# Performance work log

Hardware: AMD Instinct MI355X
Metric: run time of the kernel (lower is better)

Reference implementation:

```python
import jax, jax.numpy as jnp
import numpy as np


def setup_inputs() -> dict:
    key = jax.random.key(0)
    k1, k2, k3 = jax.random.split(key, 3)
    B, H, S, D = 2, 16, 2048, 64
    q = jax.random.normal(k1, (B, H, S, D), dtype=jnp.float32)
    k = jax.random.normal(k2, (B, H, S, D), dtype=jnp.float32)
    v = jax.random.normal(k3, (B, H, S, D), dtype=jnp.float32)
    return {"q": q, "k": k, "v": v}


def reference(q, k, v):
    # q,k,v: [B,H,S,D]; causal attention with 1/sqrt(D) scaling, fp32 softmax.
    scale = 1.0 / (q.shape[-1] ** 0.5)
    scores = jnp.einsum('bhqd,bhkd->bhqk', q * scale, k)  # [B,H,S,S]
    S = scores.shape[-1]
    causal_mask = jnp.triu(jnp.ones((S, S), dtype=bool), k=1)
    scores = jnp.where(causal_mask, -jnp.inf, scores)
    attn = jax.nn.softmax(scores.astype(jnp.float32), axis=-1).astype(q.dtype)
    output = jnp.einsum('bhqk,bhkd->bhqd', attn, v)
    # Module also returns an all-zeros attn_weights placeholder of shape [B,H,S,S]
    attn_weights = jnp.zeros(scores.shape, dtype=q.dtype)
    return (output, attn_weights)
```

## Files before the change

kernel.cpp:

```cpp
#include <hip/hip_runtime.h>


typedef __bf16 bf16x8 __attribute__((ext_vector_type(8)));
typedef float f32x4 __attribute__((ext_vector_type(4)));

#define LOG2E 1.44269504088896340736f

__device__ __forceinline__ unsigned short f2bf(float f) {
  unsigned int u = __float_as_uint(f);
  u += 0x7fffu + ((u >> 16) & 1u);
  return (unsigned short)(u >> 16);
}

__device__ __forceinline__ void block_sync_lds() {
  asm volatile("s_waitcnt lgkmcnt(0)" ::: "memory");
  __builtin_amdgcn_s_barrier();
}

constexpr int Sdim = 2048, Ddim = 64, BHn = 32;
constexpr int STiles = 16;
constexpr int LDK = 72;
constexpr int OUT0 = BHn * Sdim * Ddim;
constexpr size_t FILL_PER_BH = 1048576;

__device__ __forceinline__ int vswz_m(int d) { return ((d >> 2) ^ (d >> 5)) & 7; }

__global__ __launch_bounds__(256, 2)
void flash_causal_kernel(const float* __restrict__ Q, const float* __restrict__ K,
                         const float* __restrict__ V, float* __restrict__ out) {
  __shared__ unsigned short Klds[2][64 * LDK];
  __shared__ unsigned short Vlds[2][64 * LDK];
  __shared__ unsigned short Plds[4][2][16 * LDK];

  const int tid  = threadIdx.x;
  const int wave = tid >> 6;
  const int lane = tid & 63;
  const int quad = lane >> 4;
  const int l15  = lane & 15;

  const int bh = blockIdx.x & (BHn - 1);
  const int g  = (int)(blockIdx.x >> 5);
  const int s  = (g & 1) ? (STiles - 1) - (g >> 1) : (g >> 1);
  const int jmax = 2 * s + 1;

  const int base  = bh * Sdim * Ddim;
  const int qbase = s * 128;

  bf16x8 aq[2][2];
  #pragma unroll
  for (int f = 0; f < 2; ++f) {
    const float* qp = Q + base + (qbase + 64 * f + wave * 16 + l15) * Ddim + quad * 8;
    #pragma unroll
    for (int s2 = 0; s2 < 2; ++s2) {
      float4 a = *(const float4*)(qp + 32 * s2);
      float4 b = *(const float4*)(qp + 32 * s2 + 4);
      union { unsigned short u[8]; bf16x8 v; } u;
      u.u[0] = f2bf(a.x * 0.125f); u.u[1] = f2bf(a.y * 0.125f);
      u.u[2] = f2bf(a.z * 0.125f); u.u[3] = f2bf(a.w * 0.125f);
      u.u[4] = f2bf(b.x * 0.125f); u.u[5] = f2bf(b.y * 0.125f);
      u.u[6] = f2bf(b.z * 0.125f); u.u[7] = f2bf(b.w * 0.125f);
      aq[f][s2] = u.v;
    }
  }

  f32x4 ot[2][4];
  #pragma unroll
  for (int f = 0; f < 2; ++f)
    #pragma unroll
    for (int t = 0; t < 4; ++t) ot[f][t] = (f32x4){0.f, 0.f, 0.f, 0.f};
  float mrun[2] = {-__builtin_inff(), -__builtin_inff()};
  float lrun[2] = {0.f, 0.f};

  const float4* kg4 = (const float4*)(K + base);
  const float4* vg4 = (const float4*)(V + base);
  float4 kf[4], vf[4];

  auto ldtile = [&](int j) {
    const float4* kp = kg4 + j * 1024;
    const float4* vp = vg4 + j * 1024;
    #pragma unroll
    for (int i = 0; i < 4; ++i) { kf[i] = kp[i * 256 + tid]; vf[i] = vp[i * 256 + tid]; }
  };
  auto stage = [&](int buf) {
    #pragma unroll
    for (int i = 0; i < 4; ++i) {
      int lin = i * 256 + tid;
      int row = lin >> 4;
      int c4  = (lin & 15) << 2;
      uint2 t2;
      t2.x = (unsigned int)f2bf(kf[i].x) | ((unsigned int)f2bf(kf[i].y) << 16);
      t2.y = (unsigned int)f2bf(kf[i].z) | ((unsigned int)f2bf(kf[i].w) << 16);
      *(uint2*)&Klds[buf][row * LDK + c4] = t2;
      const int sw = vswz_m(c4) << 3;
      Vlds[buf][(c4 + 0) * LDK + (row ^ sw)] = f2bf(vf[i].x);
      Vlds[buf][(c4 + 1) * LDK + (row ^ sw)] = f2bf(vf[i].y);
      Vlds[buf][(c4 + 2) * LDK + (row ^ sw)] = f2bf(vf[i].z);
      Vlds[buf][(c4 + 3) * LDK + (row ^ sw)] = f2bf(vf[i].w);
    }
  };

  ldtile(0); stage(0); ldtile(1);

  for (int j = 0; j <= jmax; ++j) {
    block_sync_lds();
    if (j < jmax) stage((j + 1) & 1);
    if (j + 2 <= jmax) ldtile(j + 2);

    const unsigned short* Kb = Klds[j & 1];
    const unsigned short* Vb = Vlds[j & 1];
    const bool f0act = (j <= 2 * s);

    f32x4 sc[2][4];
    #pragma unroll
    for (int f = 0; f < 2; ++f)
      #pragma unroll
      for (int t = 0; t < 4; ++t) sc[f][t] = (f32x4){0.f, 0.f, 0.f, 0.f};
    __builtin_amdgcn_s_setprio(1);
    #pragma unroll
    for (int s2 = 0; s2 < 2; ++s2) {
      #pragma unroll
      for (int t = 0; t < 4; ++t) {
        bf16x8 ka = *(const bf16x8*)&Kb[(16 * t + l15) * LDK + 32 * s2 + quad * 8];
        sc[0][t] = __builtin_amdgcn_mfma_f32_16x16x32_bf16(ka, aq[0][s2], sc[0][t], 0, 0, 0);
        sc[1][t] = __builtin_amdgcn_mfma_f32_16x16x32_bf16(ka, aq[1][s2], sc[1][t], 0, 0, 0);
      }
    }
    __builtin_amdgcn_s_setprio(0);

    #pragma unroll
    for (int f = 0; f < 2; ++f) {
      if (j == 2 * s + f) {
        const int qml = wave * 16 + l15;
        #pragma unroll
        for (int t = 0; t < 4; ++t)
          #pragma unroll
          for (int r = 0; r < 4; ++r)
            if (16 * t + 4 * quad + r > qml) sc[f][t][r] = -__builtin_inff();
      }
    }

    #pragma unroll
    for (int f = 0; f < 2; ++f) {
      if (f == 0 && !f0act) continue;
      float mx = sc[f][0][0];
      #pragma unroll
      for (int t = 0; t < 4; ++t)
        #pragma unroll
        for (int r = 0; r < 4; ++r) mx = fmaxf(mx, sc[f][t][r]);
      mx = fmaxf(mx, __shfl_xor(mx, 16));
      mx = fmaxf(mx, __shfl_xor(mx, 32));
      float mn    = fmaxf(mrun[f], mx);
      float alpha = __builtin_amdgcn_exp2f((mrun[f] - mn) * LOG2E);
      float msc   = mn * LOG2E;
      mrun[f] = mn;
      float rs = 0.f;
      #pragma unroll
      for (int t = 0; t < 4; ++t)
        #pragma unroll
        for (int r = 0; r < 4; ++r) {
          float p = __builtin_amdgcn_exp2f(fmaf(sc[f][t][r], LOG2E, -msc));
          sc[f][t][r] = p;
          rs += p;
        }
      rs += __shfl_xor(rs, 16);
      rs += __shfl_xor(rs, 32);
      lrun[f] = lrun[f] * alpha + rs;
      #pragma unroll
      for (int t = 0; t < 4; ++t)
        #pragma unroll
        for (int r = 0; r < 4; ++r) ot[f][t][r] *= alpha;
      #pragma unroll
      for (int t = 0; t < 4; ++t) {
        uint2 pw;
        pw.x = (unsigned int)f2bf(sc[f][t][0]) | ((unsigned int)f2bf(sc[f][t][1]) << 16);
        pw.y = (unsigned int)f2bf(sc[f][t][2]) | ((unsigned int)f2bf(sc[f][t][3]) << 16);
        *(uint2*)&Plds[wave][f][l15 * LDK + 16 * t + 4 * quad] = pw;
      }
    }

    __builtin_amdgcn_s_setprio(1);
    #pragma unroll
    for (int s2 = 0; s2 < 2; ++s2) {
      bf16x8 pb0, pb1;
      if (f0act) pb0 = *(const bf16x8*)&Plds[wave][0][l15 * LDK + 32 * s2 + quad * 8];
      pb1 = *(const bf16x8*)&Plds[wave][1][l15 * LDK + 32 * s2 + quad * 8];
      #pragma unroll
      for (int t = 0; t < 4; ++t) {
        const int d = 16 * t + l15;
        bf16x8 va = *(const bf16x8*)&Vb[d * LDK + (((4 * s2 + quad) ^ vswz_m(d)) << 3)];
        if (f0act)
          ot[0][t] = __builtin_amdgcn_mfma_f32_16x16x32_bf16(va, pb0, ot[0][t], 0, 0, 0);
        ot[1][t] = __builtin_amdgcn_mfma_f32_16x16x32_bf16(va, pb1, ot[1][t], 0, 0, 0);
      }
    }
    __builtin_amdgcn_s_setprio(0);
  }

  #pragma unroll
  for (int f = 0; f < 2; ++f) {
    float inv = 1.0f / lrun[f];
    float* orow = out + base + (qbase + 64 * f + wave * 16 + l15) * Ddim + 4 * quad;
    #pragma unroll
    for (int t = 0; t < 4; ++t) {
      f32x4 o4;
      o4.x = ot[f][t][0] * inv; o4.y = ot[f][t][1] * inv;
      o4.z = ot[f][t][2] * inv; o4.w = ot[f][t][3] * inv;
      *(f32x4*)(orow + 16 * t) = o4;
    }
  }

  {
    const int gp = (STiles - 1) - s;
    const int w  = 2 * gp + 1;
    const size_t start_f4 = (size_t)bh * FILL_PER_BH + (size_t)4096 * (gp * gp);
    const size_t count_f4 = (size_t)4096 * w;
    f32x4 z4 = (f32x4){0.f, 0.f, 0.f, 0.f};
    f32x4* zp = (f32x4*)(out + OUT0) + start_f4;
    for (size_t i = tid; i < count_f4; i += 256)
      __builtin_nontemporal_store(z4, zp + i);
  }
}

extern "C" void kernel_launch(void* const* d_in, const int* in_sizes, int n_in,
                              void* d_out, int out_size, void* d_ws, size_t ws_size,
                              hipStream_t stream) {
  const float* q = (const float*)d_in[0];
  const float* k = (const float*)d_in[1];
  const float* v = (const float*)d_in[2];
  float* out = (float*)d_out;
  dim3 grid(BHn * STiles);
  flash_causal_kernel<<<grid, dim3(256), 0, stream>>>(q, k, v, out);
}
```

Before: 586.6 us.

## Split zero-fill into dedicated blocks interleaved with attention blocks

The grid becomes 768 blocks, and every third block only writes its contiguous share of the all-zero attention-weights output. The other two in each group run the attention tiles, so attention blocks no longer carry a trailing zero-fill tail of uneven size. Launch bounds rise to three blocks per CU, and the P scratch buffer uses a tighter stride to cut LDS use. The aim is to overlap the write-bandwidth-bound fill with compute-bound attention across CUs. The cost is possible register pressure or spills under the tighter occupancy bound.

```diff
diff --git a/kernel.cpp b/kernel.cpp
--- a/kernel.cpp
+++ b/kernel.cpp
@@ -20,26 +20,42 @@
 constexpr int Sdim = 2048, Ddim = 64, BHn = 32;
 constexpr int STiles = 16;
 constexpr int LDK = 72;
+constexpr int LDP = 68;
 constexpr int OUT0 = BHn * Sdim * Ddim;
-constexpr size_t FILL_PER_BH = 1048576;
+constexpr size_t FILL_F4_PER_BLK = 131072;
 
 __device__ __forceinline__ int vswz_m(int d) { return ((d >> 2) ^ (d >> 5)) & 7; }
 
-__global__ __launch_bounds__(256, 2)
+__global__ __launch_bounds__(256, 3)
 void flash_causal_kernel(const float* __restrict__ Q, const float* __restrict__ K,
                          const float* __restrict__ V, float* __restrict__ out) {
   __shared__ unsigned short Klds[2][64 * LDK];
   __shared__ unsigned short Vlds[2][64 * LDK];
-  __shared__ unsigned short Plds[4][2][16 * LDK];
-
-  const int tid  = threadIdx.x;
+  __shared__ unsigned short Plds[4][2][16 * LDP];
+
+  const int tid = threadIdx.x;
+  const int b   = (int)blockIdx.x;
+  const int bmod = b - (b / 3) * 3;
+
+  if (bmod == 2) {
+    const int fidx = b / 3;
+    f32x4* zp = (f32x4*)(out + OUT0) + (size_t)fidx * FILL_F4_PER_BLK;
+    const f32x4 z4 = (f32x4){0.f, 0.f, 0.f, 0.f};
+    #pragma unroll 4
+    for (size_t i = tid; i < FILL_F4_PER_BLK; i += 256)
+      __builtin_nontemporal_store(z4, zp + i);
+    return;
+  }
+
+  const int c = (b / 3) * 2 + bmod;
+
   const int wave = tid >> 6;
   const int lane = tid & 63;
   const int quad = lane >> 4;
   const int l15  = lane & 15;
 
-  const int bh = blockIdx.x & (BHn - 1);
-  const int g  = (int)(blockIdx.x >> 5);
+  const int bh = c & (BHn - 1);
+  const int g  = c >> 5;
   const int s  = (g & 1) ? (STiles - 1) - (g >> 1) : (g >> 1);
   const int jmax = 2 * s + 1;
 
@@ -53,12 +69,12 @@
     #pragma unroll
     for (int s2 = 0; s2 < 2; ++s2) {
       float4 a = *(const float4*)(qp + 32 * s2);
-      float4 b = *(const float4*)(qp + 32 * s2 + 4);
+      float4 bq = *(const float4*)(qp + 32 * s2 + 4);
       union { unsigned short u[8]; bf16x8 v; } u;
-      u.u[0] = f2bf(a.x * 0.125f); u.u[1] = f2bf(a.y * 0.125f);
-      u.u[2] = f2bf(a.z * 0.125f); u.u[3] = f2bf(a.w * 0.125f);
-      u.u[4] = f2bf(b.x * 0.125f); u.u[5] = f2bf(b.y * 0.125f);
-      u.u[6] = f2bf(b.z * 0.125f); u.u[7] = f2bf(b.w * 0.125f);
+      u.u[0] = f2bf(a.x * 0.125f);  u.u[1] = f2bf(a.y * 0.125f);
+      u.u[2] = f2bf(a.z * 0.125f);  u.u[3] = f2bf(a.w * 0.125f);
+      u.u[4] = f2bf(bq.x * 0.125f); u.u[5] = f2bf(bq.y * 0.125f);
+      u.u[6] = f2bf(bq.z * 0.125f); u.u[7] = f2bf(bq.w * 0.125f);
       aq[f][s2] = u.v;
     }
   }
@@ -174,7 +190,7 @@
         uint2 pw;
         pw.x = (unsigned int)f2bf(sc[f][t][0]) | ((unsigned int)f2bf(sc[f][t][1]) << 16);
         pw.y = (unsigned int)f2bf(sc[f][t][2]) | ((unsigned int)f2bf(sc[f][t][3]) << 16);
-        *(uint2*)&Plds[wave][f][l15 * LDK + 16 * t + 4 * quad] = pw;
+        *(uint2*)&Plds[wave][f][l15 * LDP + 16 * t + 4 * quad] = pw;
       }
     }
 
@@ -182,8 +198,8 @@
     #pragma unroll
     for (int s2 = 0; s2 < 2; ++s2) {
       bf16x8 pb0, pb1;
-      if (f0act) pb0 = *(const bf16x8*)&Plds[wave][0][l15 * LDK + 32 * s2 + quad * 8];
-      pb1 = *(const bf16x8*)&Plds[wave][1][l15 * LDK + 32 * s2 + quad * 8];
+      if (f0act) pb0 = *(const bf16x8*)&Plds[wave][0][l15 * LDP + 32 * s2 + quad * 8];
+      pb1 = *(const bf16x8*)&Plds[wave][1][l15 * LDP + 32 * s2 + quad * 8];
       #pragma unroll
       for (int t = 0; t < 4; ++t) {
         const int d = 16 * t + l15;
@@ -207,17 +223,6 @@
       o4.z = ot[f][t][2] * inv; o4.w = ot[f][t][3] * inv;
       *(f32x4*)(orow + 16 * t) = o4;
     }
-  }
-
-  {
-    const int gp = (STiles - 1) - s;
-    const int w  = 2 * gp + 1;
-    const size_t start_f4 = (size_t)bh * FILL_PER_BH + (size_t)4096 * (gp * gp);
-    const size_t count_f4 = (size_t)4096 * w;
-    f32x4 z4 = (f32x4){0.f, 0.f, 0.f, 0.f};
-    f32x4* zp = (f32x4*)(out + OUT0) + start_f4;
-    for (size_t i = tid; i < count_f4; i += 256)
-      __builtin_nontemporal_store(z4, zp + i);
   }
 }
 
@@ -228,6 +233,6 @@
   const float* k = (const float*)d_in[1];
   const float* v = (const float*)d_in[2];
   float* out = (float*)d_out;
-  dim3 grid(BHn * STiles);
+  dim3 grid(768);
   flash_causal_kernel<<<grid, dim3(256), 0, stream>>>(q, k, v, out);
 }
```

After: 654.5 us. +11.6%, slower.

## Enlarge tiles to 256-query blocks with 512 threads and 128-key tiles

Applied to the files above, without the earlier changes.

Each block now handles 256 query rows with 8 waves of 512 threads and consumes 128-key K/V tiles, so the grid shrinks to 256 blocks. The larger tiles give more reuse of each staged K/V tile and fewer barriers per key. The cost is more registers per thread (the score tile doubles) and more masked work on the diagonal. The grid now has exactly one block per CU with coarse, uneven causal work, because the interleaved load-balancing order of query tiles was dropped. This risks tail imbalance and lower occupancy.

```diff
diff --git a/kernel.cpp b/kernel.cpp
--- a/kernel.cpp
+++ b/kernel.cpp
@@ -18,19 +18,22 @@
 }
 
 constexpr int Sdim = 2048, Ddim = 64, BHn = 32;
-constexpr int STiles = 16;
+constexpr int QTiles = 8;
 constexpr int LDK = 72;
+constexpr int LDV = 136;
+constexpr int LDP = 136;
 constexpr int OUT0 = BHn * Sdim * Ddim;
 constexpr size_t FILL_PER_BH = 1048576;
+constexpr int FILL_UNIT_F4 = 16384;
 
 __device__ __forceinline__ int vswz_m(int d) { return ((d >> 2) ^ (d >> 5)) & 7; }
 
-__global__ __launch_bounds__(256, 2)
+__global__ __launch_bounds__(512, 2)
 void flash_causal_kernel(const float* __restrict__ Q, const float* __restrict__ K,
                          const float* __restrict__ V, float* __restrict__ out) {
-  __shared__ unsigned short Klds[2][64 * LDK];
-  __shared__ unsigned short Vlds[2][64 * LDK];
-  __shared__ unsigned short Plds[4][2][16 * LDK];
+  __shared__ unsigned short Klds[2][128 * LDK];
+  __shared__ unsigned short Vlds[2][64 * LDV];
+  __shared__ unsigned short Plds[8][2][16 * LDP];
 
   const int tid  = threadIdx.x;
   const int wave = tid >> 6;
@@ -38,27 +41,26 @@
   const int quad = lane >> 4;
   const int l15  = lane & 15;
 
-  const int bh = blockIdx.x & (BHn - 1);
-  const int g  = (int)(blockIdx.x >> 5);
-  const int s  = (g & 1) ? (STiles - 1) - (g >> 1) : (g >> 1);
-  const int jmax = 2 * s + 1;
+  const int bh = (int)blockIdx.x & (BHn - 1);
+  const int t  = (int)blockIdx.x >> 5;
+  const int jmax = 2 * t + 1;
 
   const int base  = bh * Sdim * Ddim;
-  const int qbase = s * 128;
+  const int qbase = t * 256;
 
   bf16x8 aq[2][2];
   #pragma unroll
   for (int f = 0; f < 2; ++f) {
-    const float* qp = Q + base + (qbase + 64 * f + wave * 16 + l15) * Ddim + quad * 8;
+    const float* qp = Q + base + (qbase + 32 * wave + 16 * f + l15) * Ddim + quad * 8;
     #pragma unroll
     for (int s2 = 0; s2 < 2; ++s2) {
       float4 a = *(const float4*)(qp + 32 * s2);
-      float4 b = *(const float4*)(qp + 32 * s2 + 4);
+      float4 bq = *(const float4*)(qp + 32 * s2 + 4);
       union { unsigned short u[8]; bf16x8 v; } u;
-      u.u[0] = f2bf(a.x * 0.125f); u.u[1] = f2bf(a.y * 0.125f);
-      u.u[2] = f2bf(a.z * 0.125f); u.u[3] = f2bf(a.w * 0.125f);
-      u.u[4] = f2bf(b.x * 0.125f); u.u[5] = f2bf(b.y * 0.125f);
-      u.u[6] = f2bf(b.z * 0.125f); u.u[7] = f2bf(b.w * 0.125f);
+      u.u[0] = f2bf(a.x * 0.125f);  u.u[1] = f2bf(a.y * 0.125f);
+      u.u[2] = f2bf(a.z * 0.125f);  u.u[3] = f2bf(a.w * 0.125f);
+      u.u[4] = f2bf(bq.x * 0.125f); u.u[5] = f2bf(bq.y * 0.125f);
+      u.u[6] = f2bf(bq.z * 0.125f); u.u[7] = f2bf(bq.w * 0.125f);
       aq[f][s2] = u.v;
     }
   }
@@ -67,7 +69,7 @@
   #pragma unroll
   for (int f = 0; f < 2; ++f)
     #pragma unroll
-    for (int t = 0; t < 4; ++t) ot[f][t] = (f32x4){0.f, 0.f, 0.f, 0.f};
+    for (int tt = 0; tt < 4; ++tt) ot[f][tt] = (f32x4){0.f, 0.f, 0.f, 0.f};
   float mrun[2] = {-__builtin_inff(), -__builtin_inff()};
   float lrun[2] = {0.f, 0.f};
 
@@ -76,15 +78,15 @@
   float4 kf[4], vf[4];
 
   auto ldtile = [&](int j) {
-    const float4* kp = kg4 + j * 1024;
-    const float4* vp = vg4 + j * 1024;
-    #pragma unroll
-    for (int i = 0; i < 4; ++i) { kf[i] = kp[i * 256 + tid]; vf[i] = vp[i * 256 + tid]; }
+    const float4* kp = kg4 + j * 2048;
+    const float4* vp = vg4 + j * 2048;
+    #pragma unroll
+    for (int i = 0; i < 4; ++i) { kf[i] = kp[i * 512 + tid]; vf[i] = vp[i * 512 + tid]; }
   };
   auto stage = [&](int buf) {
     #pragma unroll
     for (int i = 0; i < 4; ++i) {
-      int lin = i * 256 + tid;
+      int lin = i * 512 + tid;
       int row = lin >> 4;
       int c4  = (lin & 15) << 2;
       uint2 t2;
@@ -92,10 +94,10 @@
       t2.y = (unsigned int)f2bf(kf[i].z) | ((unsigned int)f2bf(kf[i].w) << 16);
       *(uint2*)&Klds[buf][row * LDK + c4] = t2;
       const int sw = vswz_m(c4) << 3;
-      Vlds[buf][(c4 + 0) * LDK + (row ^ sw)] = f2bf(vf[i].x);
-      Vlds[buf][(c4 + 1) * LDK + (row ^ sw)] = f2bf(vf[i].y);
-      Vlds[buf][(c4 + 2) * LDK + (row ^ sw)] = f2bf(vf[i].z);
-      Vlds[buf][(c4 + 3) * LDK + (row ^ sw)] = f2bf(vf[i].w);
+      Vlds[buf][(c4 + 0) * LDV + (row ^ sw)] = f2bf(vf[i].x);
+      Vlds[buf][(c4 + 1) * LDV + (row ^ sw)] = f2bf(vf[i].y);
+      Vlds[buf][(c4 + 2) * LDV + (row ^ sw)] = f2bf(vf[i].z);
+      Vlds[buf][(c4 + 3) * LDV + (row ^ sw)] = f2bf(vf[i].w);
     }
   };
 
@@ -108,45 +110,43 @@
 
     const unsigned short* Kb = Klds[j & 1];
     const unsigned short* Vb = Vlds[j & 1];
-    const bool f0act = (j <= 2 * s);
-
-    f32x4 sc[2][4];
+
+    f32x4 sc[2][8];
     #pragma unroll
     for (int f = 0; f < 2; ++f)
       #pragma unroll
-      for (int t = 0; t < 4; ++t) sc[f][t] = (f32x4){0.f, 0.f, 0.f, 0.f};
+      for (int tt = 0; tt < 8; ++tt) sc[f][tt] = (f32x4){0.f, 0.f, 0.f, 0.f};
     __builtin_amdgcn_s_setprio(1);
     #pragma unroll
     for (int s2 = 0; s2 < 2; ++s2) {
       #pragma unroll
-      for (int t = 0; t < 4; ++t) {
-        bf16x8 ka = *(const bf16x8*)&Kb[(16 * t + l15) * LDK + 32 * s2 + quad * 8];
-        sc[0][t] = __builtin_amdgcn_mfma_f32_16x16x32_bf16(ka, aq[0][s2], sc[0][t], 0, 0, 0);
-        sc[1][t] = __builtin_amdgcn_mfma_f32_16x16x32_bf16(ka, aq[1][s2], sc[1][t], 0, 0, 0);
+      for (int tt = 0; tt < 8; ++tt) {
+        bf16x8 ka = *(const bf16x8*)&Kb[(16 * tt + l15) * LDK + 32 * s2 + quad * 8];
+        sc[0][tt] = __builtin_amdgcn_mfma_f32_16x16x32_bf16(ka, aq[0][s2], sc[0][tt], 0, 0, 0);
+        sc[1][tt] = __builtin_amdgcn_mfma_f32_16x16x32_bf16(ka, aq[1][s2], sc[1][tt], 0, 0, 0);
       }
     }
     __builtin_amdgcn_s_setprio(0);
 
-    #pragma unroll
-    for (int f = 0; f < 2; ++f) {
-      if (j == 2 * s + f) {
-        const int qml = wave * 16 + l15;
-        #pragma unroll
-        for (int t = 0; t < 4; ++t)
+    if (j >= 2 * t) {
+      #pragma unroll
+      for (int f = 0; f < 2; ++f) {
+        const int qml = 32 * wave + 16 * f + l15 - ((j - 2 * t) << 7);
+        #pragma unroll
+        for (int tt = 0; tt < 8; ++tt)
           #pragma unroll
           for (int r = 0; r < 4; ++r)
-            if (16 * t + 4 * quad + r > qml) sc[f][t][r] = -__builtin_inff();
+            if (16 * tt + 4 * quad + r > qml) sc[f][tt][r] = -__builtin_inff();
       }
     }
 
     #pragma unroll
     for (int f = 0; f < 2; ++f) {
-      if (f == 0 && !f0act) continue;
       float mx = sc[f][0][0];
       #pragma unroll
-      for (int t = 0; t < 4; ++t)
-        #pragma unroll
-        for (int r = 0; r < 4; ++r) mx = fmaxf(mx, sc[f][t][r]);
+      for (int tt = 0; tt < 8; ++tt)
+        #pragma unroll
+        for (int r = 0; r < 4; ++r) mx = fmaxf(mx, sc[f][tt][r]);
       mx = fmaxf(mx, __shfl_xor(mx, 16));
       mx = fmaxf(mx, __shfl_xor(mx, 32));
       float mn    = fmaxf(mrun[f], mx);
@@ -155,42 +155,40 @@
       mrun[f] = mn;
       float rs = 0.f;
       #pragma unroll
-      for (int t = 0; t < 4; ++t)
+      for (int tt = 0; tt < 8; ++tt)
         #pragma unroll
         for (int r = 0; r < 4; ++r) {
-          float p = __builtin_amdgcn_exp2f(fmaf(sc[f][t][r], LOG2E, -msc));
-          sc[f][t][r] = p;
+          float p = __builtin_amdgcn_exp2f(fmaf(sc[f][tt][r], LOG2E, -msc));
+          sc[f][tt][r] = p;
           rs += p;
         }
       rs += __shfl_xor(rs, 16);
       rs += __shfl_xor(rs, 32);
       lrun[f] = lrun[f] * alpha + rs;
       #pragma unroll
-      for (int t = 0; t < 4; ++t)
-        #pragma unroll
-        for (int r = 0; r < 4; ++r) ot[f][t][r] *= alpha;
-      #pragma unroll
-      for (int t = 0; t < 4; ++t) {
+      for (int tt = 0; tt < 4; ++tt)
+        #pragma unroll
+        for (int r = 0; r < 4; ++r) ot[f][tt][r] *= alpha;
+      #pragma unroll
+      for (int tt = 0; tt < 8; ++tt) {
         uint2 pw;
-        pw.x = (unsigned int)f2bf(sc[f][t][0]) | ((unsigned int)f2bf(sc[f][t][1]) << 16);
-        pw.y = (unsigned int)f2bf(sc[f][t][2]) | ((unsigned int)f2bf(sc[f][t][3]) << 16);
-        *(uint2*)&Plds[wave][f][l15 * LDK + 16 * t + 4 * quad] = pw;
+        pw.x = (unsigned int)f2bf(sc[f][tt][0]) | ((unsigned int)f2bf(sc[f][tt][1]) << 16);
+        pw.y = (unsigned int)f2bf(sc[f][tt][2]) | ((unsigned int)f2bf(sc[f][tt][3]) << 16);
+        *(uint2*)&Plds[wave][f][l15 * LDP + 16 * tt + 4 * quad] = pw;
       }
     }
 
     __builtin_amdgcn_s_setprio(1);
     #pragma unroll
-    for (int s2 = 0; s2 < 2; ++s2) {
-      bf16x8 pb0, pb1;
-      if (f0act) pb0 = *(const bf16x8*)&Plds[wave][0][l15 * LDK + 32 * s2 + quad * 8];
-      pb1 = *(const bf16x8*)&Plds[wave][1][l15 * LDK + 32 * s2 + quad * 8];
-      #pragma unroll
-      for (int t = 0; t < 4; ++t) {
-        const int d = 16 * t + l15;
-        bf16x8 va = *(const bf16x8*)&Vb[d * LDK + (((4 * s2 + quad) ^ vswz_m(d)) << 3)];
-        if (f0act)
-          ot[0][t] = __builtin_amdgcn_mfma_f32_16x16x32_bf16(va, pb0, ot[0][t], 0, 0, 0);
-        ot[1][t] = __builtin_amdgcn_mfma_f32_16x16x32_bf16(va, pb1, ot[1][t], 0, 0, 0);
+    for (int ks = 0; ks < 4; ++ks) {
+      bf16x8 pb0 = *(const bf16x8*)&Plds[wave][0][l15 * LDP + 32 * ks + quad * 8];
+      bf16x8 pb1 = *(const bf16x8*)&Plds[wave][1][l15 * LDP + 32 * ks + quad * 8];
+      #pragma unroll
+      for (int tt = 0; tt < 4; ++tt) {
+        const int d = 16 * tt + l15;
+        bf16x8 va = *(const bf16x8*)&Vb[d * LDV + (((4 * ks + quad) ^ vswz_m(d)) << 3)];
+        ot[0][tt] = __builtin_amdgcn_mfma_f32_16x16x32_bf16(va, pb0, ot[0][tt], 0, 0, 0);
+        ot[1][tt] = __builtin_amdgcn_mfma_f32_16x16x32_bf16(va, pb1, ot[1][tt], 0, 0, 0);
       }
     }
     __builtin_amdgcn_s_setprio(0);
@@ -199,24 +197,23 @@
   #pragma unroll
   for (int f = 0; f < 2; ++f) {
     float inv = 1.0f / lrun[f];
-    float* orow = out + base + (qbase + 64 * f + wave * 16 + l15) * Ddim + 4 * quad;
-    #pragma unroll
-    for (int t = 0; t < 4; ++t) {
+    float* orow = out + base + (qbase + 32 * wave + 16 * f + l15) * Ddim + 4 * quad;
+    #pragma unroll
+    for (int tt = 0; tt < 4; ++tt) {
       f32x4 o4;
-      o4.x = ot[f][t][0] * inv; o4.y = ot[f][t][1] * inv;
-      o4.z = ot[f][t][2] * inv; o4.w = ot[f][t][3] * inv;
-      *(f32x4*)(orow + 16 * t) = o4;
+      o4.x = ot[f][tt][0] * inv; o4.y = ot[f][tt][1] * inv;
+      o4.z = ot[f][tt][2] * inv; o4.w = ot[f][tt][3] * inv;
+      *(f32x4*)(orow + 16 * tt) = o4;
     }
   }
 
   {
-    const int gp = (STiles - 1) - s;
-    const int w  = 2 * gp + 1;
-    const size_t start_f4 = (size_t)bh * FILL_PER_BH + (size_t)4096 * (gp * gp);
-    const size_t count_f4 = (size_t)4096 * w;
+    const int r = (QTiles - 1) - t;
+    const size_t start_f4 = (size_t)bh * FILL_PER_BH + (size_t)FILL_UNIT_F4 * (r * r);
+    const size_t count_f4 = (size_t)FILL_UNIT_F4 * (2 * r + 1);
     f32x4 z4 = (f32x4){0.f, 0.f, 0.f, 0.f};
     f32x4* zp = (f32x4*)(out + OUT0) + start_f4;
-    for (size_t i = tid; i < count_f4; i += 256)
+    for (size_t i = tid; i < count_f4; i += 512)
       __builtin_nontemporal_store(z4, zp + i);
   }
 }
@@ -228,6 +225,6 @@
   const float* k = (const float*)d_in[1];
   const float* v = (const float*)d_in[2];
   float* out = (float*)d_out;
-  dim3 grid(BHn * STiles);
-  flash_causal_kernel<<<grid, dim3(256), 0, stream>>>(q, k, v, out);
-}
+  dim3 grid(BHn * QTiles);
+  flash_causal_kernel<<<grid, dim3(512), 0, stream>>>(q, k, v, out);
+}
```

Result: no change. 598.2 us (+2.0%).
